# Optimization experiments

Hardware: AMD Instinct MI355X
Metric: run time of the kernel (lower is better)

## Reference

```python
import jax, jax.numpy as jnp
import numpy as np
from math import isqrt

NUM_HEADS = 8
EPS = 1e-12  # torch F.normalize default eps


def _l2_normalize_seq(t):
    # normalize over the sequence axis (dim=-2), matching F.normalize(t, dim=-2)
    n = jnp.sqrt(jnp.sum(t * t, axis=-2, keepdims=True))
    return t / jnp.maximum(n, EPS)


def setup_inputs() -> dict:
    key = jax.random.key(0)
    ks = jax.random.split(key, 7)
    B, L, C = 8, 4096, 384
    s = 0.02
    return {
        "x": jax.random.normal(ks[0], (B, L, C), jnp.float32),
        "qkv_w": jax.random.normal(ks[1], (3 * C, C), jnp.float32) * s,
        "qkv_b": jax.random.normal(ks[2], (3 * C,), jnp.float32) * s,
        "proj_w": jax.random.normal(ks[3], (C, C), jnp.float32) * s,
        "proj_b": jax.random.normal(ks[4], (C,), jnp.float32) * s,
        "temperature": jnp.ones((NUM_HEADS, 1, 1), jnp.float32),
        "conv_w": jax.random.normal(ks[5], (C, 1, 3, 3), jnp.float32) * s,
        "conv_b": jax.random.normal(ks[6], (C,), jnp.float32) * s,
    }


def reference(x, qkv_w, qkv_b, proj_w, proj_b, temperature, conv_w, conv_b):
    B, L, C = x.shape
    h = NUM_HEADS
    d = C // h
    H = W = isqrt(L)

    # qkv projection -> (3, B, h, L, d)
    qkv = (x @ qkv_w.T + qkv_b).reshape(B, L, 3, h, d).transpose(2, 0, 3, 1, 4)
    q, k, v = qkv[0], qkv[1], qkv[2]

    # L2 normalize q, k over sequence axis
    q = _l2_normalize_seq(q)
    k = _l2_normalize_seq(k)

    # LePE: depthwise 3x3 conv on v in image layout (B, C, H, W)
    v_img = v.transpose(0, 1, 3, 2).reshape(B, C, H, W)
    lepe = jax.lax.conv_general_dilated(
        v_img, conv_w, window_strides=(1, 1), padding=((1, 1), (1, 1)),
        feature_group_count=C,
        dimension_numbers=("NCHW", "OIHW", "NCHW"),
    ) + conv_b[None, :, None, None]
    lepe = lepe.reshape(B, h, d, L).transpose(0, 1, 3, 2)  # (B, h, L, d)

    # linear attention: attn = (k^T v) * temperature, shape (B, h, d, d)
    attn = jnp.einsum("bhld,bhle->bhde", k, v) * temperature
    out = jnp.einsum("bhld,bhde->bhle", q, attn) + lepe  # (B, h, L, d)

    out = out.transpose(0, 2, 1, 3).reshape(B, L, C)
    out = out @ proj_w.T + proj_b
    return (out, attn)
```

## Files before the change

### kernel.cpp

```cpp
#include <hip/hip_runtime.h>
#include <hip/hip_bf16.h>


typedef __bf16 bf16x8 __attribute__((ext_vector_type(8)));
typedef float f32x4 __attribute__((ext_vector_type(4)));

__device__ inline __bf16 f2b(float f) {
    __hip_bfloat16 h = __float2bfloat16(f);
    __bf16 r; __builtin_memcpy(&r, &h, 2); return r;
}
__device__ inline float b2f(__hip_bfloat16 h) { return __bfloat162float(h); }
__device__ inline float b2f(__bf16 v) {
    __hip_bfloat16 h; __builtin_memcpy(&h, &v, 2); return __bfloat162float(h);
}

__device__ inline bf16x8 load8(const __hip_bfloat16* p) {
    uint4 v = *(const uint4*)p;
    bf16x8 r; __builtin_memcpy(&r, &v, 16); return r;
}
__device__ inline bf16x8 load8(const float* p) {
    float4 a = *(const float4*)p;
    float4 b = *(const float4*)(p + 4);
    bf16x8 r;
    r[0] = f2b(a.x); r[1] = f2b(a.y); r[2] = f2b(a.z); r[3] = f2b(a.w);
    r[4] = f2b(b.x); r[5] = f2b(b.y); r[6] = f2b(b.z); r[7] = f2b(b.w);
    return r;
}

__device__ inline void storef(float* p, float v) { *p = v; }
__device__ inline void storef(__hip_bfloat16* p, float v) { *p = __float2bfloat16(v); }

__device__ inline void gl_lds16(const __hip_bfloat16* g, __hip_bfloat16* l) {
    __builtin_amdgcn_global_load_lds(
        (const __attribute__((address_space(1))) void*)g,
        (__attribute__((address_space(3))) void*)l,
        16, 0, 0);
}

__global__ __launch_bounds__(256) void cvt_kernel(
    const float* __restrict__ x,  __hip_bfloat16* __restrict__ xb,
    const float* __restrict__ qw, __hip_bfloat16* __restrict__ qwb,
    const float* __restrict__ pw, __hip_bfloat16* __restrict__ pwb)
{
    int blk = blockIdx.x;
    const float* src; __hip_bfloat16* dst; int base;
    if (blk < 6144)      { src = x;  dst = xb;  base = blk; }
    else if (blk < 6360) { src = qw; dst = qwb; base = blk - 6144; }
    else                 { src = pw; dst = pwb; base = blk - 6360; }
    int i = base * 256 + threadIdx.x;
    bf16x8 v = load8(src + (size_t)i * 8);
    *(bf16x8*)(dst + (size_t)i * 8) = v;
}

template <typename TO>
__global__ __launch_bounds__(256) void gemm_bf16_nt(
    const __hip_bfloat16* __restrict__ A,
    const __hip_bfloat16* __restrict__ Bw,
    const float* __restrict__ bias,
    TO* __restrict__ C,
    int N, int K, int NXT,
    float* __restrict__ sq)
{
    __shared__ __hip_bfloat16 As[128 * 32];
    __shared__ __hip_bfloat16 Bs[128 * 32];
    const int t = threadIdx.x;
    const int w = t >> 6, lane = t & 63;
    const int r16 = lane & 15, quad = lane >> 4;
    const int bx  = blockIdx.x;
    const int xcd = bx & 7, seq = bx >> 3;
    const int n_t = seq % NXT, m_t = seq / NXT;
    const int m0 = (xcd + 8 * m_t) * 128;
    const int n0 = n_t * 128;
    const int wm = w >> 1, wn = w & 1;
    const int srow = lane >> 2;
    const int scol = (lane & 3) * 8;

    f32x4 acc[4][4];
    #pragma unroll
    for (int mi = 0; mi < 4; ++mi)
        #pragma unroll
        for (int ni = 0; ni < 4; ++ni)
            acc[mi][ni] = (f32x4){0.f, 0.f, 0.f, 0.f};

    for (int k0 = 0; k0 < K; k0 += 32) {
        #pragma unroll
        for (int p = 0; p < 2; ++p) {
            int row = w * 32 + p * 16 + srow;
            gl_lds16(A  + (size_t)(m0 + row) * K + k0 + scol, &As[row * 32 + scol]);
            gl_lds16(Bw + (size_t)(n0 + row) * K + k0 + scol, &Bs[row * 32 + scol]);
        }
        __syncthreads();
        bf16x8 af[4], bfr[4];
        #pragma unroll
        for (int mi = 0; mi < 4; ++mi)
            af[mi] = *(const bf16x8*)&As[(wm * 64 + mi * 16 + r16) * 32 + quad * 8];
        #pragma unroll
        for (int ni = 0; ni < 4; ++ni)
            bfr[ni] = *(const bf16x8*)&Bs[(wn * 64 + ni * 16 + r16) * 32 + quad * 8];
        #pragma unroll
        for (int mi = 0; mi < 4; ++mi)
            #pragma unroll
            for (int ni = 0; ni < 4; ++ni)
                acc[mi][ni] = __builtin_amdgcn_mfma_f32_16x16x32_bf16(af[mi], bfr[ni], acc[mi][ni], 0, 0, 0);
        __syncthreads();
    }

    #pragma unroll
    for (int ni = 0; ni < 4; ++ni) {
        int col = n0 + wn * 64 + ni * 16 + r16;
        float bv = bias[col];
        float s = 0.f;
        #pragma unroll
        for (int mi = 0; mi < 4; ++mi) {
            #pragma unroll
            for (int reg = 0; reg < 4; ++reg) {
                int row = m0 + wm * 64 + mi * 16 + quad * 4 + reg;
                float o = acc[mi][ni][reg] + bv;
                storef(&C[(size_t)row * N + col], o);
                s += o * o;
            }
        }
        if (sq != nullptr && col < 768) {
            s += __shfl_xor(s, 16);
            s += __shfl_xor(s, 32);
            if (quad == 0) {
                int b = m0 >> 12;
                atomicAdd(&sq[b * 768 + col], s);
            }
        }
    }
}

__global__ void invnorm_kernel(const float* __restrict__ sumsq, float* __restrict__ invn)
{
    int i = blockIdx.x * 256 + threadIdx.x;
    if (i < 6144) invn[i] = 1.f / fmaxf(sqrtf(sumsq[i]), 1e-12f);
}

__global__ __launch_bounds__(256) void ktv_mfma_kernel(
    const __hip_bfloat16* __restrict__ qkv, float* __restrict__ G)
{
    __shared__ __hip_bfloat16 kT[4][48][40];
    __shared__ __hip_bfloat16 vT[4][48][40];
    __shared__ float red[4][48][49];

    const int bh = blockIdx.y; const int b = bh >> 3; const int h = bh & 7;
    const int lbase = blockIdx.x * 1024;
    const int t = threadIdx.x;
    const int w = t >> 6, lane = t & 63;
    const int r16 = lane & 15, quad = lane >> 4;

    f32x4 acc[3][3];
    #pragma unroll
    for (int mi = 0; mi < 3; ++mi)
        #pragma unroll
        for (int ni = 0; ni < 3; ++ni)
            acc[mi][ni] = (f32x4){0.f, 0.f, 0.f, 0.f};

    const int mat  = t & 1;
    const int lrow = t >> 1;
    const int tile = lrow >> 5, l_in = lrow & 31;
    const __hip_bfloat16* src = qkv + 384 + mat * 384 + h * 48;
    __hip_bfloat16* dstT = (mat ? &vT[0][0][0] : &kT[0][0][0]) + ((size_t)tile * 48 * 40 + l_in);

    for (int it = 0; it < 8; ++it) {
        const int l0 = lbase + it * 128;
        const __hip_bfloat16* p = src + (size_t)(b * 4096 + l0 + lrow) * 1152;
        __hip_bfloat16 row[48];
        #pragma unroll
        for (int j = 0; j < 6; ++j) {
            uint4 v = *(const uint4*)(p + j * 8);
            __builtin_memcpy(&row[j * 8], &v, 16);
        }
        #pragma unroll
        for (int d = 0; d < 48; ++d)
            dstT[d * 40] = row[d];
        __syncthreads();

        bf16x8 af[3], bfr[3];
        #pragma unroll
        for (int mi = 0; mi < 3; ++mi)
            af[mi] = *(const bf16x8*)&kT[w][mi * 16 + r16][quad * 8];
        #pragma unroll
        for (int ni = 0; ni < 3; ++ni)
            bfr[ni] = *(const bf16x8*)&vT[w][ni * 16 + r16][quad * 8];
        #pragma unroll
        for (int mi = 0; mi < 3; ++mi)
            #pragma unroll
            for (int ni = 0; ni < 3; ++ni)
                acc[mi][ni] = __builtin_amdgcn_mfma_f32_16x16x32_bf16(af[mi], bfr[ni], acc[mi][ni], 0, 0, 0);
        __syncthreads();
    }

    #pragma unroll
    for (int mi = 0; mi < 3; ++mi)
        #pragma unroll
        for (int ni = 0; ni < 3; ++ni)
            #pragma unroll
            for (int reg = 0; reg < 4; ++reg)
                red[w][mi * 16 + quad * 4 + reg][ni * 16 + r16] = acc[mi][ni][reg];
    __syncthreads();

    float* Gb = G + (size_t)bh * 2304;
    for (int cell = t; cell < 2304; cell += 256) {
        int row = cell / 48, col = cell % 48;
        float s = red[0][row][col] + red[1][row][col] + red[2][row][col] + red[3][row][col];
        atomicAdd(&Gb[cell], s);
    }
}

__global__ void scale_attn_kernel(
    const float* __restrict__ G, const float* __restrict__ invn,
    const float* __restrict__ temp,
    float* __restrict__ attn_out, float* __restrict__ attn2)
{
    int bh = blockIdx.x; int b = bh >> 3; int h = bh & 7;
    float tf = temp[h];
    int t = threadIdx.x;
    for (int e = t; e < 2304; e += 256) {
        int dk = e / 48;
        float ink = invn[b * 768 + 384 + h * 48 + dk];
        float inq = invn[b * 768 + h * 48 + dk];
        float av  = G[(size_t)bh * 2304 + e] * ink * tf;
        attn_out[(size_t)bh * 2304 + e] = av;
        attn2[(size_t)bh * 2304 + e]    = av * inq;
    }
}

__global__ __launch_bounds__(256) void qattn_lepe_mfma(
    const __hip_bfloat16* __restrict__ qkv, const float* __restrict__ attn2,
    const float* __restrict__ conv_w, const float* __restrict__ conv_b,
    __hip_bfloat16* __restrict__ y)
{
    __shared__ __attribute__((aligned(16))) char smem[26624];
    __hip_bfloat16 (*qs)[72]  = (__hip_bfloat16 (*)[72])smem;
    __hip_bfloat16 (*a2s)[72] = (__hip_bfloat16 (*)[72])(smem + 18432);
    float (*ys)[52]           = (float (*)[52])smem;
    __shared__ __hip_bfloat16 vs[4][64][48];
    __shared__ float cwT[9][48];
    __shared__ float cb[48];

    const int bh = blockIdx.y; const int b = bh >> 3; const int h = bh & 7;
    const int yi0 = blockIdx.x * 2;
    const int l0  = yi0 * 64;
    const int t = threadIdx.x;
    const int w = t >> 6, lane = t & 63;
    const int r16 = lane & 15, quad = lane >> 4;

    const __hip_bfloat16* qbase = qkv + (size_t)(b * 4096 + l0) * 1152 + h * 48;
    #pragma unroll
    for (int i = 0; i < 3; ++i) {
        int chunk = t + i * 256;
        int row = chunk / 6, cg = chunk % 6;
        *(bf16x8*)&qs[row][cg * 8] = load8(qbase + (size_t)row * 1152 + cg * 8);
    }
    *(bf16x8*)&qs[t >> 1][48 + (t & 1) * 8] = (bf16x8)0;

    const float* a2g = attn2 + (size_t)bh * 2304;
    for (int i = t; i < 3072; i += 256) {
        int e = i >> 6, dd = i & 63;
        float val = (dd < 48) ? a2g[dd * 48 + e] : 0.f;
        a2s[e][dd] = __float2bfloat16(val);
    }

    const __hip_bfloat16* vbase = qkv + (size_t)b * 4096 * 1152 + 768 + h * 48;
    #pragma unroll
    for (int i = 0; i < 6; ++i) {
        int chunk = t + i * 256;
        int r = chunk / 384, rem = chunk % 384;
        int xx = rem / 6, cg = rem % 6;
        int yy = yi0 - 1 + r;
        bf16x8 v = (yy >= 0 && yy < 64)
            ? load8(vbase + (size_t)(yy * 64 + xx) * 1152 + cg * 8)
            : (bf16x8)0;
        *(bf16x8*)&vs[r][xx][cg * 8] = v;
    }

    for (int i = t; i < 432; i += 256)
        cwT[i / 48][i % 48] = conv_w[(h * 48 + (i % 48)) * 9 + (i / 48)];
    if (t < 48) cb[t] = conv_b[h * 48 + t];
    __syncthreads();

    f32x4 acc[2][3];
    #pragma unroll
    for (int mi = 0; mi < 2; ++mi)
        #pragma unroll
        for (int ni = 0; ni < 3; ++ni)
            acc[mi][ni] = (f32x4){0.f, 0.f, 0.f, 0.f};
    #pragma unroll
    for (int ks = 0; ks < 2; ++ks) {
        int kb = ks * 32 + quad * 8;
        bf16x8 af[2], bfr[3];
        #pragma unroll
        for (int mi = 0; mi < 2; ++mi)
            af[mi] = *(const bf16x8*)&qs[w * 32 + mi * 16 + r16][kb];
        #pragma unroll
        for (int ni = 0; ni < 3; ++ni)
            bfr[ni] = *(const bf16x8*)&a2s[ni * 16 + r16][kb];
        #pragma unroll
        for (int mi = 0; mi < 2; ++mi)
            #pragma unroll
            for (int ni = 0; ni < 3; ++ni)
                acc[mi][ni] = __builtin_amdgcn_mfma_f32_16x16x32_bf16(af[mi], bfr[ni], acc[mi][ni], 0, 0, 0);
    }
    __syncthreads();

    #pragma unroll
    for (int mi = 0; mi < 2; ++mi)
        #pragma unroll
        for (int ni = 0; ni < 3; ++ni)
            #pragma unroll
            for (int reg = 0; reg < 4; ++reg)
                ys[w * 32 + mi * 16 + quad * 4 + reg][ni * 16 + r16] = acc[mi][ni][reg];
    __syncthreads();

    __hip_bfloat16* ybase = y + (size_t)(b * 4096 + l0) * 384 + h * 48;
    #pragma unroll
    for (int i = 0; i < 3; ++i) {
        int g = t + i * 256;
        int l_in = g / 6, cg = g % 6, e0 = cg * 8;
        int xi = l_in & 63, vr0 = l_in >> 6;
        float o[8];
        #pragma unroll
        for (int j = 0; j < 8; ++j) o[j] = ys[l_in][e0 + j] + cb[e0 + j];
        #pragma unroll
        for (int dy = 0; dy < 3; ++dy) {
            #pragma unroll
            for (int dx = 0; dx < 3; ++dx) {
                int xx = xi + dx - 1;
                if (xx < 0 || xx > 63) continue;
                bf16x8 vv = *(const bf16x8*)&vs[vr0 + dy][xx][e0];
                const float* cwp = &cwT[dy * 3 + dx][e0];
                #pragma unroll
                for (int j = 0; j < 8; ++j) o[j] += b2f(vv[j]) * cwp[j];
            }
        }
        __hip_bfloat16 ob[8];
        #pragma unroll
        for (int j = 0; j < 8; ++j) ob[j] = __float2bfloat16(o[j]);
        uint4 pk; __builtin_memcpy(&pk, ob, 16);
        *(uint4*)(ybase + (size_t)l_in * 384 + e0) = pk;
    }
}

extern "C" void kernel_launch(void* const* d_in, const int* in_sizes, int n_in,
                              void* d_out, int out_size, void* d_ws, size_t ws_size,
                              hipStream_t stream)
{
    const float* x      = (const float*)d_in[0];
    const float* qkv_w  = (const float*)d_in[1];
    const float* qkv_b  = (const float*)d_in[2];
    const float* proj_w = (const float*)d_in[3];
    const float* proj_b = (const float*)d_in[4];
    const float* temp   = (const float*)d_in[5];
    const float* conv_w = (const float*)d_in[6];
    const float* conv_b = (const float*)d_in[7];

    char* ws = (char*)d_ws;
    __hip_bfloat16* qkv = (__hip_bfloat16*)(ws);
    __hip_bfloat16* yb  = (__hip_bfloat16*)(ws + 75497472);
    float* sumsq = (float*)(ws + 100663296);
    float* G     = (float*)(ws + 100687872);
    float* invn  = (float*)(ws + 101277696);
    float* attn2 = (float*)(ws + 101302272);
    __hip_bfloat16* x_bf16  = yb;
    __hip_bfloat16* qkv_wb  = (__hip_bfloat16*)(ws + 101892096);
    __hip_bfloat16* proj_wb = (__hip_bfloat16*)(ws + 102776832);

    float* out      = (float*)d_out;
    float* attn_out = out + 12582912;

    (void)hipMemsetAsync(ws + 100663296, 0, 614400, stream);

    cvt_kernel<<<6432, 256, 0, stream>>>(x, x_bf16, qkv_w, qkv_wb, proj_w, proj_wb);
    gemm_bf16_nt<__hip_bfloat16><<<2304, 256, 0, stream>>>(
        x_bf16, qkv_wb, qkv_b, qkv, 1152, 384, 9, sumsq);
    invnorm_kernel<<<24, 256, 0, stream>>>(sumsq, invn);
    ktv_mfma_kernel<<<dim3(4, 64), 256, 0, stream>>>(qkv, G);
    scale_attn_kernel<<<64, 256, 0, stream>>>(G, invn, temp, attn_out, attn2);
    qattn_lepe_mfma<<<dim3(32, 64), 256, 0, stream>>>(qkv, attn2, conv_w, conv_b, yb);
    gemm_bf16_nt<float><<<768, 256, 0, stream>>>(
        yb, proj_wb, proj_b, out, 384, 384, 3, nullptr);
}
```

Baseline: 256.8 us.

## Retile GEMM to 128x64 with K-chunk 64, XOR-swizzled LDS, compile-time K

Result: faster. 231.0 us (-10.1%).

```diff
diff --git a/kernel.cpp b/kernel.cpp
--- a/kernel.cpp
+++ b/kernel.cpp
@@ -52,17 +52,17 @@
     *(bf16x8*)(dst + (size_t)i * 8) = v;
 }
 
-template <typename TO>
+template <typename TO, int KC, bool FUSE_SQ>
 __global__ __launch_bounds__(256) void gemm_bf16_nt(
     const __hip_bfloat16* __restrict__ A,
     const __hip_bfloat16* __restrict__ Bw,
     const float* __restrict__ bias,
     TO* __restrict__ C,
-    int N, int K, int NXT,
+    int N, int NXT,
     float* __restrict__ sq)
 {
-    __shared__ __hip_bfloat16 As[128 * 32];
-    __shared__ __hip_bfloat16 Bs[128 * 32];
+    __shared__ __hip_bfloat16 As[128 * 64];
+    __shared__ __hip_bfloat16 Bs[64 * 64];
     const int t = threadIdx.x;
     const int w = t >> 6, lane = t & 63;
     const int r16 = lane & 15, quad = lane >> 4;
@@ -70,44 +70,64 @@
     const int xcd = bx & 7, seq = bx >> 3;
     const int n_t = seq % NXT, m_t = seq / NXT;
     const int m0 = (xcd + 8 * m_t) * 128;
-    const int n0 = n_t * 128;
+    const int n0 = n_t * 64;
     const int wm = w >> 1, wn = w & 1;
-    const int srow = lane >> 2;
-    const int scol = (lane & 3) * 8;
-
-    f32x4 acc[4][4];
+
+    f32x4 acc[4][2];
     #pragma unroll
     for (int mi = 0; mi < 4; ++mi)
         #pragma unroll
-        for (int ni = 0; ni < 4; ++ni)
+        for (int ni = 0; ni < 2; ++ni)
             acc[mi][ni] = (f32x4){0.f, 0.f, 0.f, 0.f};
 
-    for (int k0 = 0; k0 < K; k0 += 32) {
+    for (int k0 = 0; k0 < KC; k0 += 64) {
+        #pragma unroll
+        for (int p = 0; p < 4; ++p) {
+            int c = p * 64 + lane;
+            int rl = c >> 3;
+            int cc = (c & 7) ^ (rl & 7);
+            gl_lds16(A + (size_t)(m0 + w * 32 + rl) * KC + k0 + cc * 8,
+                     &As[(w * 256 + c) * 8]);
+        }
         #pragma unroll
         for (int p = 0; p < 2; ++p) {
-            int row = w * 32 + p * 16 + srow;
-            gl_lds16(A  + (size_t)(m0 + row) * K + k0 + scol, &As[row * 32 + scol]);
-            gl_lds16(Bw + (size_t)(n0 + row) * K + k0 + scol, &Bs[row * 32 + scol]);
+            int c = p * 64 + lane;
+            int rl = c >> 3;
+            int cc = (c & 7) ^ (rl & 7);
+            gl_lds16(Bw + (size_t)(n0 + w * 16 + rl) * KC + k0 + cc * 8,
+                     &Bs[(w * 128 + c) * 8]);
         }
         __syncthreads();
-        bf16x8 af[4], bfr[4];
-        #pragma unroll
-        for (int mi = 0; mi < 4; ++mi)
-            af[mi] = *(const bf16x8*)&As[(wm * 64 + mi * 16 + r16) * 32 + quad * 8];
-        #pragma unroll
-        for (int ni = 0; ni < 4; ++ni)
-            bfr[ni] = *(const bf16x8*)&Bs[(wn * 64 + ni * 16 + r16) * 32 + quad * 8];
-        #pragma unroll
-        for (int mi = 0; mi < 4; ++mi)
-            #pragma unroll
-            for (int ni = 0; ni < 4; ++ni)
-                acc[mi][ni] = __builtin_amdgcn_mfma_f32_16x16x32_bf16(af[mi], bfr[ni], acc[mi][ni], 0, 0, 0);
+        bf16x8 af[4][2], bfr[2][2];
+        #pragma unroll
+        for (int ks = 0; ks < 2; ++ks) {
+            #pragma unroll
+            for (int mi = 0; mi < 4; ++mi) {
+                int row = wm * 64 + mi * 16 + r16;
+                int pc  = (ks * 4 + quad) ^ (r16 & 7);
+                af[mi][ks] = *(const bf16x8*)&As[row * 64 + pc * 8];
+            }
+            #pragma unroll
+            for (int ni = 0; ni < 2; ++ni) {
+                int row = wn * 32 + ni * 16 + r16;
+                int pc  = (ks * 4 + quad) ^ (r16 & 7);
+                bfr[ni][ks] = *(const bf16x8*)&Bs[row * 64 + pc * 8];
+            }
+        }
+        #pragma unroll
+        for (int ks = 0; ks < 2; ++ks)
+            #pragma unroll
+            for (int mi = 0; mi < 4; ++mi)
+                #pragma unroll
+                for (int ni = 0; ni < 2; ++ni)
+                    acc[mi][ni] = __builtin_amdgcn_mfma_f32_16x16x32_bf16(
+                        af[mi][ks], bfr[ni][ks], acc[mi][ni], 0, 0, 0);
         __syncthreads();
     }
 
     #pragma unroll
-    for (int ni = 0; ni < 4; ++ni) {
-        int col = n0 + wn * 64 + ni * 16 + r16;
+    for (int ni = 0; ni < 2; ++ni) {
+        int col = n0 + wn * 32 + ni * 16 + r16;
         float bv = bias[col];
         float s = 0.f;
         #pragma unroll
@@ -120,12 +140,14 @@
                 s += o * o;
             }
         }
-        if (sq != nullptr && col < 768) {
-            s += __shfl_xor(s, 16);
-            s += __shfl_xor(s, 32);
-            if (quad == 0) {
-                int b = m0 >> 12;
-                atomicAdd(&sq[b * 768 + col], s);
+        if constexpr (FUSE_SQ) {
+            if (col < 768) {
+                s += __shfl_xor(s, 16);
+                s += __shfl_xor(s, 32);
+                if (quad == 0) {
+                    int b = m0 >> 12;
+                    atomicAdd(&sq[b * 768 + col], s);
+                }
             }
         }
     }
@@ -373,12 +395,12 @@
     (void)hipMemsetAsync(ws + 100663296, 0, 614400, stream);
 
     cvt_kernel<<<6432, 256, 0, stream>>>(x, x_bf16, qkv_w, qkv_wb, proj_w, proj_wb);
-    gemm_bf16_nt<__hip_bfloat16><<<2304, 256, 0, stream>>>(
-        x_bf16, qkv_wb, qkv_b, qkv, 1152, 384, 9, sumsq);
+    gemm_bf16_nt<__hip_bfloat16, 384, true><<<4608, 256, 0, stream>>>(
+        x_bf16, qkv_wb, qkv_b, qkv, 1152, 18, sumsq);
     invnorm_kernel<<<24, 256, 0, stream>>>(sumsq, invn);
     ktv_mfma_kernel<<<dim3(4, 64), 256, 0, stream>>>(qkv, G);
     scale_attn_kernel<<<64, 256, 0, stream>>>(G, invn, temp, attn_out, attn2);
     qattn_lepe_mfma<<<dim3(32, 64), 256, 0, stream>>>(qkv, attn2, conv_w, conv_b, yb);
-    gemm_bf16_nt<float><<<768, 256, 0, stream>>>(
-        yb, proj_wb, proj_b, out, 384, 384, 3, nullptr);
-}
+    gemm_bf16_nt<float, 384, false><<<1536, 256, 0, stream>>>(
+        yb, proj_wb, proj_b, out, 384, 6, nullptr);
+}
```
